# Kernel optimization log

Measured on AMD Instinct MI355X. Metric: run time of the kernel, lower is better.

Reference implementation:

```python
import jax, jax.numpy as jnp
import numpy as np

NEG_INF = -1.0e9  # matches masked_fill value in the torch module


def setup_inputs() -> dict:
    key = jax.random.key(0)
    ks = jax.random.split(key, 6)
    B, N, H, D, A = 64, 2048, 512, 512, 512
    h = jax.random.normal(ks[0], (B, H), dtype=jnp.float32)
    enc_mem = jax.random.normal(ks[1], (B, N, D), dtype=jnp.float32)
    enc_mask = jax.random.randint(ks[2], (B, N), 0, 2, dtype=jnp.int32)
    # nn.Linear weights are (out_features, in_features); scale like default init
    W_h = jax.random.normal(ks[3], (A, H), dtype=jnp.float32) / np.sqrt(H)
    W_e = jax.random.normal(ks[4], (A, D), dtype=jnp.float32) / np.sqrt(D)
    v = jax.random.normal(ks[5], (A,), dtype=jnp.float32) / np.sqrt(A)
    return {"h": h, "enc_mem": enc_mem, "enc_mask": enc_mask,
            "W_h": W_h, "W_e": W_e, "v": v}


def reference(h, enc_mem, enc_mask, W_h, W_e, v):
    # energy: (B, N, A) = tanh(W_h h [broadcast over N] + W_e enc_mem)
    proj_h = jnp.einsum('bh,ah->ba', h, W_h)            # (B, A)
    proj_e = jnp.einsum('bnd,ad->bna', enc_mem, W_e)    # (B, N, A)
    energy = jnp.tanh(proj_h[:, None, :] + proj_e)      # (B, N, A)
    scores = jnp.einsum('bna,a->bn', energy, v)         # (B, N)
    scores = jnp.where(enc_mask == 0, NEG_INF, scores)
    alpha = jax.nn.softmax(scores, axis=-1)             # (B, N)
    context = jnp.einsum('bn,bnd->bd', alpha, enc_mem)  # (B, D)
    return (context, alpha)
```

## Files before the change

### kernel.cpp

```cpp
#include <hip/hip_runtime.h>
#include <hip/hip_bf16.h>
#include <cstdint>
#include <cstddef>

#define NEG_INF (-1.0e9f)

typedef __attribute__((ext_vector_type(8))) short bf16x8;
typedef __attribute__((ext_vector_type(4))) float f32x4;

constexpr int BB = 64;
constexpr int NN = 2048;
constexpr int HH = 512;
constexpr int DD = 512;
constexpr int AA = 512;

__device__ __forceinline__ float fast_rcp(float x) {
#if __has_builtin(__builtin_amdgcn_rcpf)
  return __builtin_amdgcn_rcpf(x);
#else
  return 1.f / x;
#endif
}

__device__ __forceinline__ float fast_tanh(float x) {
  float e = __expf(2.f * fabsf(x));
  float t = 1.f - 2.f * fast_rcp(e + 1.f);
  return copysignf(t, x);
}

__device__ __forceinline__ bf16x8 pack8(const float4& lo, const float4& hi) {
  __hip_bfloat162 a = __float22bfloat162_rn(float2{lo.x, lo.y});
  __hip_bfloat162 b = __float22bfloat162_rn(float2{lo.z, lo.w});
  __hip_bfloat162 c = __float22bfloat162_rn(float2{hi.x, hi.y});
  __hip_bfloat162 d = __float22bfloat162_rn(float2{hi.z, hi.w});
  union { unsigned int w[4]; bf16x8 v; } u;
  __builtin_memcpy(&u.w[0], &a, 4);
  __builtin_memcpy(&u.w[1], &b, 4);
  __builtin_memcpy(&u.w[2], &c, 4);
  __builtin_memcpy(&u.w[3], &d, 4);
  return u.v;
}

__global__ __launch_bounds__(256)
void we_cast_kernel(const float* __restrict__ We, unsigned short* __restrict__ web) {
  int i = (blockIdx.x * 256 + threadIdx.x) * 8;
  if (i >= AA * DD) return;
  float4 s0 = *(const float4*)(We + i);
  float4 s1 = *(const float4*)(We + i + 4);
  *(bf16x8*)(web + i) = pack8(s0, s1);
}

__global__ __launch_bounds__(256)
void proj_h_kernel(const float* __restrict__ h, const float* __restrict__ Wh,
                   float* __restrict__ ph) {
  __shared__ float hL[HH];
  const int b = blockIdx.x;
  hL[threadIdx.x]       = h[b * HH + threadIdx.x];
  hL[threadIdx.x + 256] = h[b * HH + threadIdx.x + 256];
  __syncthreads();
  const int a = blockIdx.y * 256 + threadIdx.x;
  const float4* wr = (const float4*)(Wh + (size_t)a * HH);
  float acc = 0.f;
  #pragma unroll 4
  for (int j = 0; j < HH / 4; ++j) {
    float4 w = wr[j];
    acc += w.x * hL[4*j] + w.y * hL[4*j+1] + w.z * hL[4*j+2] + w.w * hL[4*j+3];
  }
  ph[b * AA + a] = acc;
}

__global__ __launch_bounds__(512, 2)
void scores_fullk(const float* __restrict__ enc, const unsigned short* __restrict__ web,
                  const float* __restrict__ ph, const float* __restrict__ vvec,
                  float* __restrict__ scores) {
  constexpr int RR  = 128;
  constexpr int CK  = 128;
  constexpr int LDK = 136;

  __shared__ unsigned short As[2][RR * LDK];
  __shared__ float sred[4][RR];

  const int tid  = threadIdx.x;
  const int lane = tid & 63;
  const int wid  = tid >> 6;
  const int wr   = wid >> 2;
  const int wc   = wid & 3;
  const int c    = lane & 15;
  const int quad = lane >> 4;

  const int r0 = blockIdx.x * RR;
  const int b  = r0 >> 11;

  const int srow = (tid * 8) >> 7;
  const int scol = (tid * 8) & 127;
  const float* encBase = enc + (size_t)r0 * DD;

  float4 lo[4], hi[4];

  auto LOADREGS = [&](int kc) {
    #pragma unroll
    for (int s = 0; s < 4; ++s) {
      const float* p = encBase + (size_t)(srow + s * 32) * DD + kc * CK + scol;
      lo[s] = *(const float4*)p;
      hi[s] = *(const float4*)(p + 4);
    }
  };
  auto WRITE = [&](int buf) {
    #pragma unroll
    for (int s = 0; s < 4; ++s)
      *(bf16x8*)&As[buf][(srow + s * 32) * LDK + scol] = pack8(lo[s], hi[s]);
  };

  const unsigned short* bBase = web + ((size_t)(wc * 128 + c)) * DD + quad * 8;

  float pp[8], vv[8];
  #pragma unroll
  for (int j = 0; j < 8; ++j) {
    const int col = wc * 128 + j * 16 + c;
    pp[j] = ph[b * AA + col];
    vv[j] = vvec[col];
  }

  f32x4 acc[4][8];
  #pragma unroll
  for (int i = 0; i < 4; ++i)
    #pragma unroll
    for (int j = 0; j < 8; ++j)
      acc[i][j] = (f32x4){0.f, 0.f, 0.f, 0.f};

  LOADREGS(0);
  WRITE(0);
  __syncthreads();

  #pragma unroll
  for (int kc = 0; kc < 4; ++kc) {
    const int cur = kc & 1;
    if (kc < 3) LOADREGS(kc + 1);

    const unsigned short* aB = &As[cur][(wr * 64 + c) * LDK + quad * 8];
    const int kglob = kc * CK;
    #pragma unroll
    for (int k0 = 0; k0 < CK; k0 += 32) {
      bf16x8 bfr[8];
      #pragma unroll
      for (int j = 0; j < 8; ++j)
        bfr[j] = *(const bf16x8*)(bBase + (size_t)(j * 16) * DD + kglob + k0);
      bf16x8 af[4];
      #pragma unroll
      for (int i = 0; i < 4; ++i)
        af[i] = *(const bf16x8*)(aB + i * 16 * LDK + k0);
      #pragma unroll
      for (int i = 0; i < 4; ++i)
        #pragma unroll
        for (int j = 0; j < 8; ++j)
          acc[i][j] = __builtin_amdgcn_mfma_f32_16x16x32_bf16(af[i], bfr[j], acc[i][j], 0, 0, 0);
    }

    if (kc < 3) WRITE(cur ^ 1);
    __syncthreads();
  }

  #pragma unroll
  for (int i = 0; i < 4; ++i) {
    #pragma unroll
    for (int r = 0; r < 4; ++r) {
      float p = 0.f;
      #pragma unroll
      for (int j = 0; j < 8; ++j)
        p += vv[j] * fast_tanh(acc[i][j][r] + pp[j]);
      p += __shfl_xor(p, 1, 64);
      p += __shfl_xor(p, 2, 64);
      p += __shfl_xor(p, 4, 64);
      p += __shfl_xor(p, 8, 64);
      if (c == 0) sred[wc][wr * 64 + i * 16 + quad * 4 + r] = p;
    }
  }
  __syncthreads();
  if (tid < RR)
    scores[r0 + tid] = sred[0][tid] + sred[1][tid] + sred[2][tid] + sred[3][tid];
}

__global__ __launch_bounds__(256)
void softmax_kernel(const float* __restrict__ scores, const int* __restrict__ mask,
                    float* __restrict__ alpha) {
  const int b = blockIdx.x, tid = threadIdx.x;
  const int base = b * NN;
  float vals[8];
  float mx = -3.4e38f;
  #pragma unroll
  for (int i = 0; i < 8; ++i) {
    int n = tid + 256 * i;
    float s = scores[base + n];
    if (mask[base + n] == 0) s = NEG_INF;
    vals[i] = s;
    mx = fmaxf(mx, s);
  }
  #pragma unroll
  for (int o = 32; o; o >>= 1) mx = fmaxf(mx, __shfl_xor(mx, o, 64));
  __shared__ float w4[4];
  if ((tid & 63) == 0) w4[tid >> 6] = mx;
  __syncthreads();
  mx = fmaxf(fmaxf(w4[0], w4[1]), fmaxf(w4[2], w4[3]));
  float sum = 0.f;
  #pragma unroll
  for (int i = 0; i < 8; ++i) { vals[i] = __expf(vals[i] - mx); sum += vals[i]; }
  #pragma unroll
  for (int o = 32; o; o >>= 1) sum += __shfl_xor(sum, o, 64);
  __shared__ float s4[4];
  if ((tid & 63) == 0) s4[tid >> 6] = sum;
  __syncthreads();
  sum = s4[0] + s4[1] + s4[2] + s4[3];
  float inv = 1.f / sum;
  #pragma unroll
  for (int i = 0; i < 8; ++i) alpha[base + tid + 256 * i] = vals[i] * inv;
}

__global__ __launch_bounds__(128)
void context_part(const float* __restrict__ enc, const float* __restrict__ alpha,
                  float* __restrict__ cpart) {
  const int b  = blockIdx.x;
  const int nc = blockIdx.y;
  const int t  = threadIdx.x;
  __shared__ float aL[64];
  if (t < 64) aL[t] = alpha[b * NN + nc * 64 + t];
  __syncthreads();
  const float* ep = enc + ((size_t)b * NN + nc * 64) * DD + t * 4;
  float4 a0 = {0.f, 0.f, 0.f, 0.f}, a1 = {0.f, 0.f, 0.f, 0.f};
  #pragma unroll 4
  for (int n = 0; n < 64; n += 2) {
    float4 e0 = *(const float4*)(ep + (size_t)n * DD);
    float4 e1 = *(const float4*)(ep + (size_t)(n + 1) * DD);
    float s0 = aL[n], s1 = aL[n + 1];
    a0.x += s0 * e0.x; a0.y += s0 * e0.y; a0.z += s0 * e0.z; a0.w += s0 * e0.w;
    a1.x += s1 * e1.x; a1.y += s1 * e1.y; a1.z += s1 * e1.z; a1.w += s1 * e1.w;
  }
  a0.x += a1.x; a0.y += a1.y; a0.z += a1.z; a0.w += a1.w;
  *(float4*)(cpart + ((size_t)(b * 32 + nc)) * DD + t * 4) = a0;
}

__global__ __launch_bounds__(256)
void context_reduce(const float* __restrict__ cpart, float* __restrict__ ctx) {
  const int i = blockIdx.x * 256 + threadIdx.x;
  const int b = i >> 9, d = i & 511;
  float s = 0.f;
  #pragma unroll
  for (int nc = 0; nc < 32; ++nc) s += cpart[((size_t)(b * 32 + nc)) * DD + d];
  ctx[i] = s;
}

extern "C" void kernel_launch(void* const* d_in, const int* in_sizes, int n_in,
                              void* d_out, int out_size, void* d_ws, size_t ws_size,
                              hipStream_t stream) {
  const float* h    = (const float*)d_in[0];
  const float* enc  = (const float*)d_in[1];
  const int*   mask = (const int*)d_in[2];
  const float* Wh   = (const float*)d_in[3];
  const float* We   = (const float*)d_in[4];
  const float* v    = (const float*)d_in[5];

  float* out   = (float*)d_out;
  float* ctx   = out;
  float* alpha = out + BB * DD;

  char* w = (char*)d_ws;
  unsigned short* web = (unsigned short*)w;
  float* ph     = (float*)(w + (size_t)AA * DD * 2);
  float* scores = ph + BB * AA;
  float* cpart  = scores + BB * NN;

  we_cast_kernel<<<(AA * DD / 8 + 255) / 256, 256, 0, stream>>>(We, web);
  proj_h_kernel<<<dim3(BB, 2), 256, 0, stream>>>(h, Wh, ph);
  scores_fullk<<<(BB * NN) / 128, 512, 0, stream>>>(enc, web, ph, v, scores);
  softmax_kernel<<<BB, 256, 0, stream>>>(scores, mask, alpha);
  context_part<<<dim3(BB, 32), 128, 0, stream>>>(enc, alpha, cpart);
  context_reduce<<<(BB * DD) / 256, 256, 0, stream>>>(cpart, ctx);
  (void)in_sizes; (void)n_in; (void)out_size; (void)ws_size;
}
```

Before: 550.4 us.

## Pre-swizzle bf16 W_e into MFMA fragment tiles, raise occupancy, widen context loop

The cast kernel now writes W_e in a tiled layout where each 16x32 MFMA B-fragment is stored as 512 contiguous bf16 values. The scores kernel can then fetch each B fragment with one fully coalesced 1KB wavefront load instead of strided row reads. Launch bounds for the scores kernel go from 2 to 4 blocks per CU, which caps registers per thread and risks spilling the 32 accumulator tiles. The context partial kernel unrolls to four rows per iteration with four accumulators, giving more loads in flight.

```diff
diff --git a/kernel.cpp b/kernel.cpp
--- a/kernel.cpp
+++ b/kernel.cpp
@@ -43,11 +43,15 @@
 
 __global__ __launch_bounds__(256)
 void we_cast_kernel(const float* __restrict__ We, unsigned short* __restrict__ web) {
-  int i = (blockIdx.x * 256 + threadIdx.x) * 8;
-  if (i >= AA * DD) return;
-  float4 s0 = *(const float4*)(We + i);
-  float4 s1 = *(const float4*)(We + i + 4);
-  *(bf16x8*)(web + i) = pack8(s0, s1);
+  const int gid  = blockIdx.x * 256 + threadIdx.x;
+  const int l    = gid & 63;
+  const int tile = gid >> 6;
+  const int jc   = tile >> 4;
+  const int kg   = tile & 15;
+  const float* src = We + (size_t)(jc * 16 + (l & 15)) * DD + kg * 32 + (l >> 4) * 8;
+  float4 s0 = *(const float4*)src;
+  float4 s1 = *(const float4*)(src + 4);
+  *(bf16x8*)(web + (size_t)tile * 512 + l * 8) = pack8(s0, s1);
 }
 
 __global__ __launch_bounds__(256)
@@ -69,7 +73,7 @@
   ph[b * AA + a] = acc;
 }
 
-__global__ __launch_bounds__(512, 2)
+__global__ __launch_bounds__(512, 4)
 void scores_fullk(const float* __restrict__ enc, const unsigned short* __restrict__ web,
                   const float* __restrict__ ph, const float* __restrict__ vvec,
                   float* __restrict__ scores) {
@@ -111,7 +115,7 @@
       *(bf16x8*)&As[buf][(srow + s * 32) * LDK + scol] = pack8(lo[s], hi[s]);
   };
 
-  const unsigned short* bBase = web + ((size_t)(wc * 128 + c)) * DD + quad * 8;
+  const unsigned short* bTile = web + (size_t)(wc * 8) * 16 * 512 + (lane << 3);
 
   float pp[8], vv[8];
   #pragma unroll
@@ -138,13 +142,14 @@
     if (kc < 3) LOADREGS(kc + 1);
 
     const unsigned short* aB = &As[cur][(wr * 64 + c) * LDK + quad * 8];
-    const int kglob = kc * CK;
+    const int kg0 = kc * (CK / 32);
     #pragma unroll
     for (int k0 = 0; k0 < CK; k0 += 32) {
+      const int kg = kg0 + (k0 >> 5);
       bf16x8 bfr[8];
       #pragma unroll
       for (int j = 0; j < 8; ++j)
-        bfr[j] = *(const bf16x8*)(bBase + (size_t)(j * 16) * DD + kglob + k0);
+        bfr[j] = *(const bf16x8*)(bTile + ((size_t)(j * 16 + kg) << 9));
       bf16x8 af[4];
       #pragma unroll
       for (int i = 0; i < 4; ++i)
@@ -226,15 +231,23 @@
   __syncthreads();
   const float* ep = enc + ((size_t)b * NN + nc * 64) * DD + t * 4;
   float4 a0 = {0.f, 0.f, 0.f, 0.f}, a1 = {0.f, 0.f, 0.f, 0.f};
+  float4 a2 = {0.f, 0.f, 0.f, 0.f}, a3 = {0.f, 0.f, 0.f, 0.f};
   #pragma unroll 4
-  for (int n = 0; n < 64; n += 2) {
+  for (int n = 0; n < 64; n += 4) {
     float4 e0 = *(const float4*)(ep + (size_t)n * DD);
     float4 e1 = *(const float4*)(ep + (size_t)(n + 1) * DD);
-    float s0 = aL[n], s1 = aL[n + 1];
+    float4 e2 = *(const float4*)(ep + (size_t)(n + 2) * DD);
+    float4 e3 = *(const float4*)(ep + (size_t)(n + 3) * DD);
+    float s0 = aL[n], s1 = aL[n + 1], s2 = aL[n + 2], s3 = aL[n + 3];
     a0.x += s0 * e0.x; a0.y += s0 * e0.y; a0.z += s0 * e0.z; a0.w += s0 * e0.w;
     a1.x += s1 * e1.x; a1.y += s1 * e1.y; a1.z += s1 * e1.z; a1.w += s1 * e1.w;
-  }
-  a0.x += a1.x; a0.y += a1.y; a0.z += a1.z; a0.w += a1.w;
+    a2.x += s2 * e2.x; a2.y += s2 * e2.y; a2.z += s2 * e2.z; a2.w += s2 * e2.w;
+    a3.x += s3 * e3.x; a3.y += s3 * e3.y; a3.z += s3 * e3.z; a3.w += s3 * e3.w;
+  }
+  a0.x += a1.x + a2.x + a3.x;
+  a0.y += a1.y + a2.y + a3.y;
+  a0.z += a1.z + a2.z + a3.z;
+  a0.w += a1.w + a2.w + a3.w;
   *(float4*)(cpart + ((size_t)(b * 32 + nc)) * DD + t * 4) = a0;
 }
 
@@ -268,7 +281,7 @@
   float* scores = ph + BB * AA;
   float* cpart  = scores + BB * NN;
 
-  we_cast_kernel<<<(AA * DD / 8 + 255) / 256, 256, 0, stream>>>(We, web);
+  we_cast_kernel<<<(AA * DD / 8) / 256, 256, 0, stream>>>(We, web);
   proj_h_kernel<<<dim3(BB, 2), 256, 0, stream>>>(h, Wh, ph);
   scores_fullk<<<(BB * NN) / 128, 512, 0, stream>>>(enc, web, ph, v, scores);
   softmax_kernel<<<BB, 256, 0, stream>>>(scores, mask, alpha);
```

New measurement: 1.312 ms. +138.4%, slower.
